# Performance work log

Measured on AMD Instinct MI355X. Metric: run time of the kernel, lower is better.

## Reference

```python
import jax, jax.numpy as jnp
import numpy as np

N = 768
C = 256  # in_features == out_features (required by Linear(in_features+3, 1))

def _leaky(x):
    return jnp.where(x >= 0, x, 0.2 * x)

def setup_inputs() -> dict:
    key = jax.random.key(0)
    ks = jax.random.split(key, 10)
    features = jax.random.normal(ks[0], (N, C), dtype=jnp.float32)
    coordinates = jax.random.normal(ks[1], (N, 3), dtype=jnp.float32)
    adj = jax.random.uniform(ks[2], (N, N), dtype=jnp.float32)  # unused by forward, kept for signature fidelity
    # Learned params
    FC = jax.random.normal(ks[3], (C, C), dtype=jnp.float32) * (1.414 / jnp.sqrt(C))
    # Conv1d(2,1,kernel=1): weight [out=1, in=2, k=1] -> 2 scalars + bias
    fc_w = jax.random.normal(ks[4], (2,), dtype=jnp.float32) * 0.5
    fc_b = jax.random.normal(ks[5], (1,), dtype=jnp.float32) * 0.1
    sc_w = jax.random.normal(ks[6], (2,), dtype=jnp.float32) * 0.5
    sc_b = jax.random.normal(ks[7], (1,), dtype=jnp.float32) * 0.1
    # Linear(C+3, 1)
    lin_w = jax.random.normal(ks[8], (C + 3,), dtype=jnp.float32) * (1.0 / jnp.sqrt(C + 3))
    lin_b = jax.random.normal(ks[9], (1,), dtype=jnp.float32) * 0.1
    return {"features": features, "coordinates": coordinates, "adj": adj,
            "FC": FC, "fc_w": fc_w, "fc_b": fc_b, "sc_w": sc_w, "sc_b": sc_b,
            "lin_w": lin_w, "lin_b": lin_b}

def reference(features, coordinates, adj, FC, fc_w, fc_b, sc_w, sc_b, lin_w, lin_b):
    n = features.shape[0]
    f_input = features @ FC  # [N, C]
    # torch's repeat(1,N).view + repeat(N,1) builds pairs (i, j); the 1x1 Conv1d over
    # the 2 stacked channels is exactly w0*x_i + w1*x_j + b, then LeakyReLU(0.2).
    f_map = _leaky(fc_w[0] * f_input[:, None, :] + fc_w[1] * f_input[None, :, :] + fc_b[0])  # [N,N,C]
    s_map = _leaky(sc_w[0] * coordinates[:, None, :] + sc_w[1] * coordinates[None, :, :] + sc_b[0])  # [N,N,3]
    # Linear(C+3, 1) on cat([f_map, s_map], -1), then LeakyReLU -> [N, N]
    scores = _leaky(jnp.einsum('ijc,c->ij', f_map, lin_w[:f_input.shape[1]])
                    + jnp.einsum('ijk,k->ij', s_map, lin_w[f_input.shape[1]:])
                    + lin_b[0])
    attention = jax.nn.softmax(scores, axis=1)  # row softmax (dim=1)
    h_prime = attention @ f_input  # [N, C]
    return jax.nn.elu(h_prime)  # concat=True path
```

## Files before the change

kernel.cpp:

```cpp
#include <hip/hip_runtime.h>
#include <math.h>

#define NN 768
#define CC 256
#define TI 3
#define JC 256
#define NJC 3

__device__ __forceinline__ float leaky(float x) { return x >= 0.0f ? x : 0.2f * x; }

__device__ __forceinline__ float rl(float v, int l) {
    return __uint_as_float(__builtin_amdgcn_readlane(__float_as_uint(v), l));
}

__device__ __forceinline__ float waveMax(float v) {
    #pragma unroll
    for (int o = 32; o > 0; o >>= 1) v = fmaxf(v, __shfl_xor(v, o, 64));
    return v;
}
__device__ __forceinline__ float waveSum(float v) {
    #pragma unroll
    for (int o = 32; o > 0; o >>= 1) v += __shfl_xor(v, o, 64);
    return v;
}

__device__ __forceinline__ void acc_row(float4& a, float ur, float w4, const float4& gv) {
    a.x = fmaf(w4, fabsf(ur + gv.x), a.x);
    a.y = fmaf(w4, fabsf(ur + gv.y), a.y);
    a.z = fmaf(w4, fabsf(ur + gv.z), a.z);
    a.w = fmaf(w4, fabsf(ur + gv.w), a.w);
}
__device__ __forceinline__ void fma4(float4& h, float e, const float4& fv) {
    h.x = fmaf(e, fv.x, h.x);
    h.y = fmaf(e, fv.y, h.y);
    h.z = fmaf(e, fv.z, h.z);
    h.w = fmaf(e, fv.w, h.w);
}

__global__ __launch_bounds__(768) void k_prep(
    const float* __restrict__ features,
    const float* __restrict__ FC,
    const float* __restrict__ fc_w,
    const float* __restrict__ fc_b,
    const float* __restrict__ lin_w,
    float* __restrict__ f,
    float* __restrict__ g,
    float* __restrict__ D0,
    float* __restrict__ D1,
    float4* __restrict__ ut4)
{
    __shared__ float sA[TI * CC];
    __shared__ float sF[TI * CC];
    __shared__ float sredD[12], sredW[12];

    const int t  = threadIdx.x;
    const int r  = t >> 8;
    const int c  = t & 255;
    const int i0 = blockIdx.x * TI;

    sA[r * CC + c] = features[(i0 + r) * CC + c];
    __syncthreads();

    float a = 0.f;
    const float* fcp = FC + c;
    const float* ap  = sA + r * CC;
    #pragma unroll 8
    for (int k = 0; k < CC; ++k)
        a = fmaf(ap[k], fcp[k * CC], a);

    const float w1 = fc_w[1], b = fc_b[0];
    f[(i0 + r) * CC + c] = a;
    g[c * NN + i0 + r]   = fmaf(w1, a, b);
    sF[r * CC + c] = a;

    const float lw = lin_w[c];
    float dv = waveSum(lw * a);
    float wv = waveSum(lw);
    const int wid = t >> 6;
    if ((t & 63) == 0) { sredD[wid] = dv; sredW[wid] = wv; }
    __syncthreads();
    if (t < TI) {
        float D = sredD[t*4] + sredD[t*4+1] + sredD[t*4+2] + sredD[t*4+3];
        float W = sredW[t*4] + sredW[t*4+1] + sredW[t*4+2] + sredW[t*4+3];
        D0[i0 + t] = fc_w[0] * D;
        D1[i0 + t] = fmaf(w1, D, b * W);
    }
    if (t < CC) {
        const float w0 = fc_w[0];
        ut4[blockIdx.x * CC + t] = make_float4(w0 * sF[t],
                                               w0 * sF[CC + t],
                                               w0 * sF[2*CC + t],
                                               0.4f * lin_w[t]);
    }
}

__global__ __launch_bounds__(256) void k_attn(
    const float* __restrict__ f,
    const float* __restrict__ g,
    const float4* __restrict__ ut4,
    const float* __restrict__ D0,
    const float* __restrict__ D1,
    const float* __restrict__ coords,
    const float* __restrict__ sc_w,
    const float* __restrict__ sc_b,
    const float* __restrict__ lin_w,
    const float* __restrict__ lin_b,
    float* __restrict__ hp,
    float* __restrict__ Mp,
    float* __restrict__ Lp)
{
    __shared__ float  spart[4][TI][JC];
    __shared__ float  hpart[4][TI][CC];
    __shared__ float4 sredm4[4];
    __shared__ float4 sreds4[4];

    const int t    = threadIdx.x;
    const int it   = blockIdx.x & 255;
    const int jc   = blockIdx.x >> 8;
    const int i0   = it * TI;
    const int jb   = jc * JC;
    const int j    = jb + t;
    const int w    = t >> 6;
    const int lane = t & 63;

    float4 ureg = ut4[(size_t)it * CC + (w << 6) + lane];

    float4 a0 = make_float4(0.f,0.f,0.f,0.f);
    float4 a1 = a0, a2 = a0;
    const float4* gq = (const float4*)g + (size_t)(w << 6) * (NN/4) + (jb >> 2) + lane;
    #pragma unroll 8
    for (int cc = 0; cc < 64; ++cc) {
        float4 gv = gq[cc * (NN/4)];
        float u0 = rl(ureg.x, cc);
        float u1 = rl(ureg.y, cc);
        float u2 = rl(ureg.z, cc);
        float w4 = rl(ureg.w, cc);
        acc_row(a0, u0, w4, gv);
        acc_row(a1, u1, w4, gv);
        acc_row(a2, u2, w4, gv);
    }
    *(float4*)&spart[w][0][4*lane] = a0;
    *(float4*)&spart[w][1][4*lane] = a1;
    *(float4*)&spart[w][2][4*lane] = a2;
    __syncthreads();

    float accs[3];
    #pragma unroll
    for (int rr = 0; rr < TI; ++rr)
        accs[rr] = spart[0][rr][t] + spart[1][rr][t]
                 + spart[2][rr][t] + spart[3][rr][t];

    const float sw0 = sc_w[0], sw1 = sc_w[1], sb = sc_b[0], lb = lin_b[0];
    const float lw30 = lin_w[CC], lw31 = lin_w[CC+1], lw32 = lin_w[CC+2];
    const float cj0 = fmaf(sw1, coords[j*3+0], sb);
    const float cj1 = fmaf(sw1, coords[j*3+1], sb);
    const float cj2 = fmaf(sw1, coords[j*3+2], sb);
    const float d1  = D1[j];
    float scv[3];
    #pragma unroll
    for (int rr = 0; rr < TI; ++rr) {
        const int i = i0 + rr;
        float sd = lw30 * leaky(fmaf(sw0, coords[i*3+0], cj0))
                 + lw31 * leaky(fmaf(sw0, coords[i*3+1], cj1))
                 + lw32 * leaky(fmaf(sw0, coords[i*3+2], cj2));
        scv[rr] = leaky(accs[rr] + sd + 0.6f * (D0[i] + d1) + lb);
    }

    {
        float v0 = waveMax(scv[0]);
        float v1 = waveMax(scv[1]);
        float v2 = waveMax(scv[2]);
        if (lane == 0) sredm4[w] = make_float4(v0, v1, v2, 0.f);
    }
    __syncthreads();
    float m[TI];
    {
        float4 x0 = sredm4[0], x1 = sredm4[1], x2 = sredm4[2], x3 = sredm4[3];
        m[0] = fmaxf(fmaxf(x0.x, x1.x), fmaxf(x2.x, x3.x));
        m[1] = fmaxf(fmaxf(x0.y, x1.y), fmaxf(x2.y, x3.y));
        m[2] = fmaxf(fmaxf(x0.z, x1.z), fmaxf(x2.z, x3.z));
    }
    float e0 = __expf(scv[0] - m[0]);
    float e1 = __expf(scv[1] - m[1]);
    float e2 = __expf(scv[2] - m[2]);
    {
        float v0 = waveSum(e0);
        float v1 = waveSum(e1);
        float v2 = waveSum(e2);
        if (lane == 0) sreds4[w] = make_float4(v0, v1, v2, 0.f);
    }
    __syncthreads();
    if (t < TI) {
        float4 s0 = sreds4[0], s1 = sreds4[1], s2 = sreds4[2], s3 = sreds4[3];
        float l = (t == 0) ? (s0.x + s1.x + s2.x + s3.x)
                : (t == 1) ? (s0.y + s1.y + s2.y + s3.y)
                           : (s0.z + s1.z + s2.z + s3.z);
        float mm = (t == 0) ? m[0] : (t == 1) ? m[1] : m[2];
        Mp[(i0 + t) * NJC + jc] = mm;
        Lp[(i0 + t) * NJC + jc] = l;
    }

    float4 h0 = make_float4(0.f,0.f,0.f,0.f);
    float4 h1 = h0, h2 = h0;
    const float4* f4 = (const float4*)f;
    const int jsl = w * 64;
    #pragma unroll 8
    for (int jx = 0; jx < 64; ++jx) {
        float4 fv = f4[(size_t)(jb + jsl + jx) * 64 + lane];
        float se0 = rl(e0, jx);
        float se1 = rl(e1, jx);
        float se2 = rl(e2, jx);
        fma4(h0, se0, fv);
        fma4(h1, se1, fv);
        fma4(h2, se2, fv);
    }
    *(float4*)&hpart[w][0][4*lane] = h0;
    *(float4*)&hpart[w][1][4*lane] = h1;
    *(float4*)&hpart[w][2][4*lane] = h2;
    __syncthreads();

    #pragma unroll
    for (int r = 0; r < TI; ++r) {
        float h = hpart[0][r][t] + hpart[1][r][t] + hpart[2][r][t] + hpart[3][r][t];
        hp[((size_t)jc * NN + i0 + r) * CC + t] = h;
    }
}

__global__ __launch_bounds__(256) void k_comb(
    const float* __restrict__ hp,
    const float* __restrict__ Mp,
    const float* __restrict__ Lp,
    float* __restrict__ out)
{
    const int t = threadIdx.x;
    const int i = blockIdx.x;

    float m0 = Mp[i*NJC+0], m1 = Mp[i*NJC+1], m2 = Mp[i*NJC+2];
    float M  = fmaxf(fmaxf(m0, m1), m2);
    float w0 = __expf(m0 - M), w1 = __expf(m1 - M), w2 = __expf(m2 - M);
    float den = w0*Lp[i*NJC+0] + w1*Lp[i*NJC+1] + w2*Lp[i*NJC+2];
    float inv = 1.0f / den;

    float num = w0 * hp[((size_t)0*NN + i)*CC + t]
              + w1 * hp[((size_t)1*NN + i)*CC + t]
              + w2 * hp[((size_t)2*NN + i)*CC + t];
    float v = num * inv;
    out[i*CC + t] = (v > 0.f) ? v : (__expf(v) - 1.0f);
}

extern "C" void kernel_launch(void* const* d_in, const int* in_sizes, int n_in,
                              void* d_out, int out_size, void* d_ws, size_t ws_size,
                              hipStream_t stream) {
    const float* features = (const float*)d_in[0];
    const float* coords   = (const float*)d_in[1];
    const float* FC       = (const float*)d_in[3];
    const float* fc_w     = (const float*)d_in[4];
    const float* fc_b     = (const float*)d_in[5];
    const float* sc_w     = (const float*)d_in[6];
    const float* sc_b     = (const float*)d_in[7];
    const float* lin_w    = (const float*)d_in[8];
    const float* lin_b    = (const float*)d_in[9];
    float* out = (float*)d_out;

    float* f  = (float*)d_ws;
    float* g  = f  + NN*CC;
    float* D0 = g  + CC*NN;
    float* D1 = D0 + NN;
    float* Mp = D1 + NN;
    float* Lp = Mp + NN*NJC;
    float* hp = Lp + NN*NJC;
    float4* ut4;
    {
        size_t off = (size_t)((char*)(hp + (size_t)NJC*NN*CC) - (char*)d_ws);
        off = (off + 15) & ~(size_t)15;
        ut4 = (float4*)((char*)d_ws + off);
    }

    k_prep<<<NN/TI, 768, 0, stream>>>(features, FC, fc_w, fc_b, lin_w, f, g, D0, D1, ut4);
    k_attn<<<(NN/TI)*NJC, 256, 0, stream>>>(f, g, ut4, D0, D1, coords, sc_w, sc_b,
                                            lin_w, lin_b, hp, Mp, Lp);
    k_comb<<<NN, 256, 0, stream>>>(hp, Mp, Lp, out);
}
```

Baseline: 113.8 us.

## Give each wavefront its own j-chunk and drop block-level LDS reductions

Restructures the attention kernel so each of the four wavefronts owns a separate 64-column j chunk and reduces over all 256 channels itself. This removes shared-memory partial sums and block barriers for the score, softmax and aggregation stages. The number of softmax partials per row grows from 3 to 12, increasing partial-output traffic and the combine kernel's work. The g loads also become scalar per lane instead of float4.

```diff
diff --git a/kernel.cpp b/kernel.cpp
--- a/kernel.cpp
+++ b/kernel.cpp
@@ -4,8 +4,7 @@
 #define NN 768
 #define CC 256
 #define TI 3
-#define JC 256
-#define NJC 3
+#define NJC 12
 
 __device__ __forceinline__ float leaky(float x) { return x >= 0.0f ? x : 0.2f * x; }
 
@@ -24,12 +23,6 @@
     return v;
 }
 
-__device__ __forceinline__ void acc_row(float4& a, float ur, float w4, const float4& gv) {
-    a.x = fmaf(w4, fabsf(ur + gv.x), a.x);
-    a.y = fmaf(w4, fabsf(ur + gv.y), a.y);
-    a.z = fmaf(w4, fabsf(ur + gv.z), a.z);
-    a.w = fmaf(w4, fabsf(ur + gv.w), a.w);
-}
 __device__ __forceinline__ void fma4(float4& h, float e, const float4& fv) {
     h.x = fmaf(e, fv.x, h.x);
     h.y = fmaf(e, fv.y, h.y);
@@ -109,46 +102,38 @@
     float* __restrict__ Mp,
     float* __restrict__ Lp)
 {
-    __shared__ float  spart[4][TI][JC];
-    __shared__ float  hpart[4][TI][CC];
-    __shared__ float4 sredm4[4];
-    __shared__ float4 sreds4[4];
-
     const int t    = threadIdx.x;
-    const int it   = blockIdx.x & 255;
-    const int jc   = blockIdx.x >> 8;
-    const int i0   = it * TI;
-    const int jb   = jc * JC;
-    const int j    = jb + t;
     const int w    = t >> 6;
     const int lane = t & 63;
-
-    float4 ureg = ut4[(size_t)it * CC + (w << 6) + lane];
-
-    float4 a0 = make_float4(0.f,0.f,0.f,0.f);
-    float4 a1 = a0, a2 = a0;
-    const float4* gq = (const float4*)g + (size_t)(w << 6) * (NN/4) + (jb >> 2) + lane;
-    #pragma unroll 8
-    for (int cc = 0; cc < 64; ++cc) {
-        float4 gv = gq[cc * (NN/4)];
-        float u0 = rl(ureg.x, cc);
-        float u1 = rl(ureg.y, cc);
-        float u2 = rl(ureg.z, cc);
-        float w4 = rl(ureg.w, cc);
-        acc_row(a0, u0, w4, gv);
-        acc_row(a1, u1, w4, gv);
-        acc_row(a2, u2, w4, gv);
-    }
-    *(float4*)&spart[w][0][4*lane] = a0;
-    *(float4*)&spart[w][1][4*lane] = a1;
-    *(float4*)&spart[w][2][4*lane] = a2;
-    __syncthreads();
-
-    float accs[3];
-    #pragma unroll
-    for (int rr = 0; rr < TI; ++rr)
-        accs[rr] = spart[0][rr][t] + spart[1][rr][t]
-                 + spart[2][rr][t] + spart[3][rr][t];
+    const int rg   = blockIdx.x / 3;
+    const int jc   = (blockIdx.x % 3) * 4 + w;
+    const int i0   = rg * TI;
+    const int jb   = jc << 6;
+    const int j    = jb + lane;
+
+    float4 uq0 = ut4[(size_t)rg * CC +        lane];
+    float4 uq1 = ut4[(size_t)rg * CC +  64 + lane];
+    float4 uq2 = ut4[(size_t)rg * CC + 128 + lane];
+    float4 uq3 = ut4[(size_t)rg * CC + 192 + lane];
+
+    float a0 = 0.f, a1 = 0.f, a2 = 0.f;
+    const float* gp = g + j;
+    #pragma unroll
+    for (int k = 0; k < 4; ++k) {
+        float4 uq = (k == 0) ? uq0 : (k == 1) ? uq1 : (k == 2) ? uq2 : uq3;
+        const float* gk = gp + (size_t)(k << 6) * NN;
+        #pragma unroll 8
+        for (int li = 0; li < 64; ++li) {
+            float gv = gk[li * NN];
+            float w4 = rl(uq.w, li);
+            float u0 = rl(uq.x, li);
+            float u1 = rl(uq.y, li);
+            float u2 = rl(uq.z, li);
+            a0 = fmaf(w4, fabsf(u0 + gv), a0);
+            a1 = fmaf(w4, fabsf(u1 + gv), a1);
+            a2 = fmaf(w4, fabsf(u2 + gv), a2);
+        }
+    }
 
     const float sw0 = sc_w[0], sw1 = sc_w[1], sb = sc_b[0], lb = lin_b[0];
     const float lw30 = lin_w[CC], lw31 = lin_w[CC+1], lw32 = lin_w[CC+2];
@@ -156,6 +141,7 @@
     const float cj1 = fmaf(sw1, coords[j*3+1], sb);
     const float cj2 = fmaf(sw1, coords[j*3+2], sb);
     const float d1  = D1[j];
+    float accs[3] = {a0, a1, a2};
     float scv[3];
     #pragma unroll
     for (int rr = 0; rr < TI; ++rr) {
@@ -166,47 +152,27 @@
         scv[rr] = leaky(accs[rr] + sd + 0.6f * (D0[i] + d1) + lb);
     }
 
-    {
-        float v0 = waveMax(scv[0]);
-        float v1 = waveMax(scv[1]);
-        float v2 = waveMax(scv[2]);
-        if (lane == 0) sredm4[w] = make_float4(v0, v1, v2, 0.f);
-    }
-    __syncthreads();
-    float m[TI];
-    {
-        float4 x0 = sredm4[0], x1 = sredm4[1], x2 = sredm4[2], x3 = sredm4[3];
-        m[0] = fmaxf(fmaxf(x0.x, x1.x), fmaxf(x2.x, x3.x));
-        m[1] = fmaxf(fmaxf(x0.y, x1.y), fmaxf(x2.y, x3.y));
-        m[2] = fmaxf(fmaxf(x0.z, x1.z), fmaxf(x2.z, x3.z));
-    }
-    float e0 = __expf(scv[0] - m[0]);
-    float e1 = __expf(scv[1] - m[1]);
-    float e2 = __expf(scv[2] - m[2]);
-    {
-        float v0 = waveSum(e0);
-        float v1 = waveSum(e1);
-        float v2 = waveSum(e2);
-        if (lane == 0) sreds4[w] = make_float4(v0, v1, v2, 0.f);
-    }
-    __syncthreads();
-    if (t < TI) {
-        float4 s0 = sreds4[0], s1 = sreds4[1], s2 = sreds4[2], s3 = sreds4[3];
-        float l = (t == 0) ? (s0.x + s1.x + s2.x + s3.x)
-                : (t == 1) ? (s0.y + s1.y + s2.y + s3.y)
-                           : (s0.z + s1.z + s2.z + s3.z);
-        float mm = (t == 0) ? m[0] : (t == 1) ? m[1] : m[2];
-        Mp[(i0 + t) * NJC + jc] = mm;
-        Lp[(i0 + t) * NJC + jc] = l;
+    float m0 = waveMax(scv[0]);
+    float m1 = waveMax(scv[1]);
+    float m2 = waveMax(scv[2]);
+    float e0 = __expf(scv[0] - m0);
+    float e1 = __expf(scv[1] - m1);
+    float e2 = __expf(scv[2] - m2);
+    float l0 = waveSum(e0);
+    float l1 = waveSum(e1);
+    float l2 = waveSum(e2);
+    if (lane == 0) {
+        Mp[(i0+0) * NJC + jc] = m0;  Lp[(i0+0) * NJC + jc] = l0;
+        Mp[(i0+1) * NJC + jc] = m1;  Lp[(i0+1) * NJC + jc] = l1;
+        Mp[(i0+2) * NJC + jc] = m2;  Lp[(i0+2) * NJC + jc] = l2;
     }
 
     float4 h0 = make_float4(0.f,0.f,0.f,0.f);
     float4 h1 = h0, h2 = h0;
-    const float4* f4 = (const float4*)f;
-    const int jsl = w * 64;
+    const float4* f4 = (const float4*)f + (size_t)jb * 64 + lane;
     #pragma unroll 8
     for (int jx = 0; jx < 64; ++jx) {
-        float4 fv = f4[(size_t)(jb + jsl + jx) * 64 + lane];
+        float4 fv = f4[jx * 64];
         float se0 = rl(e0, jx);
         float se1 = rl(e1, jx);
         float se2 = rl(e2, jx);
@@ -214,16 +180,10 @@
         fma4(h1, se1, fv);
         fma4(h2, se2, fv);
     }
-    *(float4*)&hpart[w][0][4*lane] = h0;
-    *(float4*)&hpart[w][1][4*lane] = h1;
-    *(float4*)&hpart[w][2][4*lane] = h2;
-    __syncthreads();
-
-    #pragma unroll
-    for (int r = 0; r < TI; ++r) {
-        float h = hpart[0][r][t] + hpart[1][r][t] + hpart[2][r][t] + hpart[3][r][t];
-        hp[((size_t)jc * NN + i0 + r) * CC + t] = h;
-    }
+    float4* hpp = (float4*)(hp + ((size_t)jc * NN + i0) * CC) + lane;
+    hpp[0]      = h0;
+    hpp[64]     = h1;
+    hpp[128]    = h2;
 }
 
 __global__ __launch_bounds__(256) void k_comb(
@@ -235,15 +195,24 @@
     const int t = threadIdx.x;
     const int i = blockIdx.x;
 
-    float m0 = Mp[i*NJC+0], m1 = Mp[i*NJC+1], m2 = Mp[i*NJC+2];
-    float M  = fmaxf(fmaxf(m0, m1), m2);
-    float w0 = __expf(m0 - M), w1 = __expf(m1 - M), w2 = __expf(m2 - M);
-    float den = w0*Lp[i*NJC+0] + w1*Lp[i*NJC+1] + w2*Lp[i*NJC+2];
+    float mv[NJC];
+    #pragma unroll
+    for (int k = 0; k < NJC; ++k) mv[k] = Mp[i*NJC + k];
+    float M = mv[0];
+    #pragma unroll
+    for (int k = 1; k < NJC; ++k) M = fmaxf(M, mv[k]);
+    float wk[NJC], den = 0.f;
+    #pragma unroll
+    for (int k = 0; k < NJC; ++k) {
+        wk[k] = __expf(mv[k] - M);
+        den = fmaf(wk[k], Lp[i*NJC + k], den);
+    }
     float inv = 1.0f / den;
 
-    float num = w0 * hp[((size_t)0*NN + i)*CC + t]
-              + w1 * hp[((size_t)1*NN + i)*CC + t]
-              + w2 * hp[((size_t)2*NN + i)*CC + t];
+    float num = 0.f;
+    #pragma unroll
+    for (int k = 0; k < NJC; ++k)
+        num = fmaf(wk[k], hp[((size_t)k*NN + i)*CC + t], num);
     float v = num * inv;
     out[i*CC + t] = (v > 0.f) ? v : (__expf(v) - 1.0f);
 }
@@ -277,7 +246,7 @@
     }
 
     k_prep<<<NN/TI, 768, 0, stream>>>(features, FC, fc_w, fc_b, lin_w, f, g, D0, D1, ut4);
-    k_attn<<<(NN/TI)*NJC, 256, 0, stream>>>(f, g, ut4, D0, D1, coords, sc_w, sc_b,
-                                            lin_w, lin_b, hp, Mp, Lp);
+    k_attn<<<(NN/TI)*3, 256, 0, stream>>>(f, g, ut4, D0, D1, coords, sc_w, sc_b,
+                                          lin_w, lin_b, hp, Mp, Lp);
     k_comb<<<NN, 256, 0, stream>>>(hp, Mp, Lp, out);
 }
```

Result: slower. 125.1 us (+10.0%).
